# Performance work log

Hardware: AMD Instinct MI355X
Metric: run time of the kernel (lower is better)

## Reference

```python
import jax, jax.numpy as jnp
import numpy as np

N = 50000
E = 800000
C_IN = 32
C_OUT = 32
K = 8  # number of branch MLPs


def setup_inputs() -> dict:
    key = jax.random.key(0)
    ks = jax.random.split(key, 12)
    x = jax.random.normal(ks[0], (N, C_IN), dtype=jnp.float32)
    pos = jax.random.normal(ks[1], (N, 2), dtype=jnp.float32)
    edge_index = jax.random.randint(ks[2], (2, E), 0, N, dtype=jnp.int32)
    edge_attr = jax.random.normal(ks[3], (E, 4), dtype=jnp.float32)
    edge_weight = jax.random.uniform(ks[4], (E,), dtype=jnp.float32)
    s1 = 1.0 / np.sqrt(C_IN + 4)
    s2 = 1.0 / np.sqrt(C_OUT)
    W1 = jax.random.uniform(ks[5], (K, C_IN + 4, C_OUT), jnp.float32, -s1, s1)
    b1 = jax.random.uniform(ks[6], (K, C_OUT), jnp.float32, -s1, s1)
    W2 = jax.random.uniform(ks[7], (K, C_OUT, C_OUT), jnp.float32, -s2, s2)
    b2 = jax.random.uniform(ks[8], (K, C_OUT), jnp.float32, -s2, s2)
    sr = 1.0 / np.sqrt(C_IN)
    Wr = jax.random.uniform(ks[9], (C_IN, C_OUT), jnp.float32, -sr, sr)
    br = jax.random.uniform(ks[10], (C_OUT,), jnp.float32, -sr, sr)
    return {"x": x, "pos": pos, "edge_index": edge_index, "edge_attr": edge_attr,
            "edge_weight": edge_weight, "W1": W1, "b1": b1, "W2": W2, "b2": b2,
            "Wr": Wr, "br": br}


def reference(x, pos, edge_index, edge_attr, edge_weight, W1, b1, W2, b2, Wr, br):
    src = edge_index[0]  # j (source / neighbor)
    tgt = edge_index[1]  # i (target / aggregation index)

    # gather per-edge features
    x_i = x[tgt]                      # [E, C_IN]
    x_j = x[src]                      # [E, C_IN]
    diff = pos[src] - pos[tgt]        # [E, 2]

    # geometric branch index in [0, 8)
    con0 = (diff[:, 0] > 0).astype(jnp.int32)
    con1 = (diff[:, 1] > 0).astype(jnp.int32)
    con2 = (jnp.abs(diff[:, 0]) - jnp.abs(diff[:, 1]) > 0).astype(jnp.int32)
    idx = con0 + con1 * 2 + con2 * 4  # [E]

    m = jnp.concatenate([x_j - x_i, edge_attr], axis=1)  # [E, C_IN+4]
    # all 8 branch MLPs (Linear->ReLU->Linear->ReLU), then select per edge
    h = jax.nn.relu(jnp.einsum('ec,kcf->ekf', m, W1) + b1[None])   # [E, K, C_OUT]
    f_all = jax.nn.relu(jnp.einsum('ekf,kfg->ekg', h, W2) + b2[None])
    f = jnp.take_along_axis(f_all, idx[:, None, None], axis=1)[:, 0, :]  # [E, C_OUT]
    f = edge_weight[:, None] * f

    # scatter-mean over target nodes
    seg_sum = jax.ops.segment_sum(f, tgt, num_segments=N)
    counts = jax.ops.segment_sum(jnp.ones((f.shape[0],), f.dtype), tgt, num_segments=N)
    out = seg_sum / jnp.maximum(counts, 1.0)[:, None]

    # skip connection
    out = out + x @ Wr + br
    return out
```

## Files before the change

### kernel.cpp

```cpp
#include <hip/hip_runtime.h>

#define N_NODES 50000
#define N_EDGES 800000
#define K_BR    8
#define BCAP    131072
#define MLP_SLOTS (K_BR * BCAP)
#define SCAN_BLOCKS 196
#define BSTRIDE 1024
#define EPT 8
#define P1_BLOCKS 391
#define RB 128
#define RBE 6250

typedef _Float16 h2 __attribute__((ext_vector_type(2)));
typedef _Float16 half8 __attribute__((ext_vector_type(8)));
typedef float f32x4 __attribute__((ext_vector_type(4)));

#define MFMA(a, b, c) __builtin_amdgcn_mfma_f32_16x16x32_f16((a), (b), (c), 0, 0, 0)

#define VAL_MASK 0x3FFFFFFFu
#define FLG_A    0x40000000u
#define FLG_P    0x80000000u


__device__ __forceinline__ int branch_idx(float dx, float dy) {
    return (dx > 0.0f ? 1 : 0) + (dy > 0.0f ? 2 : 0) +
           ((fabsf(dx) - fabsf(dy)) > 0.0f ? 4 : 0);
}

__device__ __forceinline__ unsigned pk_f16pair(float a, float b) {
    h2 p; p.x = (_Float16)a; p.y = (_Float16)b;
    return __builtin_bit_cast(unsigned, p);
}

__device__ __forceinline__ unsigned short f16bits(float a) {
    _Float16 h = (_Float16)a;
    return __builtin_bit_cast(unsigned short, h);
}

__global__ void __launch_bounds__(256) rank_kernel(
    const int* __restrict__ ei, const float* __restrict__ x,
    const float* __restrict__ W1, const float* __restrict__ W2,
    unsigned short* __restrict__ rankB, unsigned short* __restrict__ cntM,
    unsigned* __restrict__ xh, uint4* __restrict__ w1f4, uint4* __restrict__ w2f4) {
    __shared__ unsigned hist[N_NODES / 2];
    int t = threadIdx.x, b = blockIdx.x;
    for (int i = t; i < N_NODES / 2; i += 256) hist[i] = 0;

    int tid = b * 256 + t;
    if (tid < 2048) {
        int L = tid & 63, fl = tid >> 6;
        int nt = fl & 1, kt = (fl >> 1) & 1, k = fl >> 2;
        int quad = L >> 4, col = L & 15;
        unsigned dw[4];
#pragma unroll
        for (int i = 0; i < 4; ++i) {
            float v0 = 0.0f, v1 = 0.0f;
            int k0 = kt * 32 + quad * 8 + 2 * i;
            if (k0 < 36)     v0 = W1[k * 1152 + k0 * 32 + nt * 16 + col];
            if (k0 + 1 < 36) v1 = W1[k * 1152 + (k0 + 1) * 32 + nt * 16 + col];
            dw[i] = pk_f16pair(v0, v1);
        }
        w1f4[tid] = make_uint4(dw[0], dw[1], dw[2], dw[3]);
    } else if (tid < 3072) {
        int u2 = tid - 2048;
        int L = u2 & 63, fl = u2 >> 6;
        int nt = fl & 1, k = fl >> 1;
        int quad = L >> 4, col = L & 15;
        unsigned dw[4];
#pragma unroll
        for (int i = 0; i < 4; ++i) {
            int k0 = quad * 8 + 2 * i;
            dw[i] = pk_f16pair(W2[k * 1024 + k0 * 32 + nt * 16 + col],
                               W2[k * 1024 + (k0 + 1) * 32 + nt * 16 + col]);
        }
        w2f4[u2] = make_uint4(dw[0], dw[1], dw[2], dw[3]);
    }

    __syncthreads();
    int eb = b * RBE;
    for (int it = 0; it < (RBE + 255) / 256; ++it) {
        int r = it * 256 + t;
        if (r < RBE) {
            int e = eb + r;
            int d = ei[N_EDGES + e];
            unsigned add = (d & 1) ? (1u << 16) : 1u;
            unsigned old = atomicAdd(&hist[d >> 1], add);
            unsigned rk = (d & 1) ? (old >> 16) : (old & 0xFFFFu);
            rankB[e] = (unsigned short)rk;
            float2 xv = ((const float2*)x)[e];
            xh[e] = pk_f16pair(xv.x, xv.y);
        }
    }
    __syncthreads();
    unsigned* cm = (unsigned*)(cntM + (size_t)b * N_NODES);
    for (int i = t; i < N_NODES / 2; i += 256) cm[i] = hist[i];
}

__global__ void colscan_kernel(const unsigned short* __restrict__ cntM,
                               unsigned short* __restrict__ blkBase,
                               int* __restrict__ cnt) {
    int d = blockIdx.x * 256 + threadIdx.x;
    if (d >= N_NODES) return;
    int acc = 0;
#pragma unroll 8
    for (int b = 0; b < RB; ++b) {
        size_t i = (size_t)b * N_NODES + d;
        int v = cntM[i];
        blkBase[i] = (unsigned short)acc;
        acc += v;
    }
    cnt[d] = acc;
}

__global__ void pass1_kernel(const int* __restrict__ ei, const float* __restrict__ pos,
                             const float* __restrict__ ea, const float* __restrict__ ew,
                             const unsigned short* __restrict__ rankB,
                             const unsigned short* __restrict__ blkBase,
                             int* __restrict__ bucketCur,
                             uint4* __restrict__ payload) {
    __shared__ int h[K_BR];
    __shared__ int base[K_BR];
    int t = threadIdx.x;
    if (t < K_BR) h[t] = 0;
    __syncthreads();

    int eBase = blockIdx.x * (256 * EPT);
    int sA[EPT], dA[EPT], krA[EPT], slA[EPT];
#pragma unroll
    for (int it = 0; it < EPT; ++it) {
        int e = eBase + it * 256 + t;
        int s = 0, d = 0, k = 0, rank = 0, slot = 0;
        if (e < N_EDGES) {
            s = ei[e]; d = ei[N_EDGES + e];
            float2 ps2 = ((const float2*)pos)[s];
            float2 pd2 = ((const float2*)pos)[d];
            k = branch_idx(ps2.x - pd2.x, ps2.y - pd2.y);
            rank = atomicAdd(&h[k], 1);
            int bb = e / RBE;
            slot = (int)blkBase[(size_t)bb * N_NODES + d] + (int)rankB[e];
        }
        sA[it] = s; dA[it] = d; krA[it] = (k << 16) | rank; slA[it] = slot;
    }
    __syncthreads();
    if (t < K_BR) base[t] = (h[t] > 0) ? atomicAdd(&bucketCur[t * BSTRIDE], h[t]) : 0;
    __syncthreads();
#pragma unroll
    for (int it = 0; it < EPT; ++it) {
        int e = eBase + it * 256 + t;
        if (e < N_EDGES) {
            int k = krA[it] >> 16, rank = krA[it] & 0xFFFF;
            float4 eav = ((const float4*)ea)[e];
            unsigned ewh = (unsigned)f16bits(ew[e]);
            int idx = (k << 17) + base[k] + rank;
            payload[idx] = make_uint4((unsigned)sA[it] | ((unsigned)dA[it] << 16),
                                      (unsigned)slA[it] | (ewh << 16),
                                      pk_f16pair(eav.x, eav.y),
                                      pk_f16pair(eav.z, eav.w));
        }
    }
}

__global__ void scan_kernel(const int* __restrict__ cnt, unsigned* __restrict__ ps,
                            int* __restrict__ nodeStart) {
    __shared__ int s[256];
    __shared__ int sh_off;
    int t = threadIdx.x, b = blockIdx.x;
    int i = b * 256 + t;
    int v = (i < N_NODES) ? cnt[i] : 0;
    s[t] = v;
    __syncthreads();
#pragma unroll
    for (int off = 1; off < 256; off <<= 1) {
        int tmp = (t >= off) ? s[t - off] : 0;
        __syncthreads();
        s[t] += tmp;
        __syncthreads();
    }
    int excl = s[t] - v;
    if (t == 255)
        atomicExch(&ps[b], (unsigned)s[255] | (b == 0 ? FLG_P : FLG_A));
    if (t == 0) sh_off = 0;
    if (t < 64 && b > 0) {
        int off = 0;
        int base = b - 1;
        for (;;) {
            int idx = base - t;
            unsigned w = 0;
            if (idx >= 0) {
                do { w = atomicOr(&ps[idx], 0u); } while (!(w & (FLG_A | FLG_P)));
            }
            bool isP = (w & FLG_P) != 0;
            unsigned long long pm = __ballot(isP);
            int firstP = pm ? (__ffsll((unsigned long long)pm) - 1) : 64;
            int contrib = (idx >= 0 && t <= firstP) ? (int)(w & VAL_MASK) : 0;
#pragma unroll
            for (int sh = 32; sh > 0; sh >>= 1) contrib += __shfl_down(contrib, sh, 64);
            contrib = __shfl(contrib, 0, 64);
            off += contrib;
            if (firstP < 64 || base - 64 < 0) break;
            base -= 64;
        }
        if (t == 0) sh_off = off;
    }
    __syncthreads();
    if (i < N_NODES) nodeStart[i] = excl + sh_off;
}

__global__ void __launch_bounds__(64) mlp_kernel(
    const uint4* __restrict__ payload,
    const unsigned* __restrict__ xh,
    const uint4* __restrict__ w1f4, const float* __restrict__ b1,
    const uint4* __restrict__ w2f4, const float* __restrict__ b2,
    const int* __restrict__ nodeStart,
    const int* __restrict__ bucketFill,
    unsigned short* __restrict__ fbuf) {
    __shared__ uint4 lds4[656];
    char* mreg = (char*)lds4;
    char* hreg = mreg + 9216;

    int t = blockIdx.x * 64 + threadIdx.x;
    int u = __builtin_amdgcn_readfirstlane(t);
    int k = u >> 17;
    int fill = bucketFill[k * BSTRIDE];
    if ((u & (BCAP - 1)) >= fill) return;
    int rel = t & (BCAP - 1);
    bool valid = rel < fill;
    int idx = (k << 17) + min(rel, fill - 1);

    int L = threadIdx.x;
    int quad = L >> 4, col = L & 15;

    uint4 pl = payload[idx];
    int s = (int)(pl.x & 0xFFFFu);
    int d = (int)(pl.x >> 16);
    _Float16 wh = __builtin_bit_cast(_Float16, (unsigned short)(pl.y >> 16));
    int slot = valid ? (nodeStart[d] + (int)(pl.y & 0xFFFFu)) : 0;

    const uint4* xj = ((const uint4*)xh) + 4 * (size_t)s;
    const uint4* xi = ((const uint4*)xh) + 4 * (size_t)d;
    uint4* mrow = (uint4*)(mreg + L * 144);
#pragma unroll
    for (int q = 0; q < 4; ++q) {
        half8 a8 = __builtin_bit_cast(half8, xj[q]);
        half8 b8 = __builtin_bit_cast(half8, xi[q]);
        half8 d8 = a8 - b8;
        mrow[q] = __builtin_bit_cast(uint4, d8);
    }
    mrow[4] = make_uint4(pl.z, pl.w, 0u, 0u);
    mrow[5] = make_uint4(0u, 0u, 0u, 0u);
    mrow[6] = make_uint4(0u, 0u, 0u, 0u);
    mrow[7] = make_uint4(0u, 0u, 0u, 0u);

    half8 B1[2][2], B2[2];
#pragma unroll
    for (int kt = 0; kt < 2; ++kt)
#pragma unroll
        for (int nt = 0; nt < 2; ++nt)
            B1[kt][nt] = __builtin_bit_cast(half8, w1f4[((k * 2 + kt) * 2 + nt) * 64 + L]);
#pragma unroll
    for (int nt = 0; nt < 2; ++nt)
        B2[nt] = __builtin_bit_cast(half8, w2f4[(k * 2 + nt) * 64 + L]);
    float b1o0 = b1[k * 32 + col],      b1o1 = b1[k * 32 + 16 + col];
    float b2o0 = b2[k * 32 + col],      b2o1 = b2[k * 32 + 16 + col];

#pragma unroll
    for (int mt = 0; mt < 4; ++mt) {
        int arow = mt * 16 + col;
        half8 a0 = __builtin_bit_cast(half8, *(const uint4*)(mreg + arow * 144 + quad * 16));
        half8 a1 = __builtin_bit_cast(half8, *(const uint4*)(mreg + arow * 144 + 64 + quad * 16));
        f32x4 c0 = {b1o0, b1o0, b1o0, b1o0};
        f32x4 c1 = {b1o1, b1o1, b1o1, b1o1};
        c0 = MFMA(a0, B1[0][0], c0);
        c0 = MFMA(a1, B1[1][0], c0);
        c1 = MFMA(a0, B1[0][1], c1);
        c1 = MFMA(a1, B1[1][1], c1);
#pragma unroll
        for (int r = 0; r < 4; ++r) {
            int er = quad * 4 + r;
            *(unsigned short*)(hreg + er * 80 + col * 2)        = f16bits(fmaxf(c0[r], 0.0f));
            *(unsigned short*)(hreg + er * 80 + (16 + col) * 2) = f16bits(fmaxf(c1[r], 0.0f));
        }
        half8 ah = __builtin_bit_cast(half8, *(const uint4*)(hreg + col * 80 + quad * 16));
        f32x4 d0 = {b2o0, b2o0, b2o0, b2o0};
        f32x4 d1 = {b2o1, b2o1, b2o1, b2o1};
        d0 = MFMA(ah, B2[0], d0);
        d1 = MFMA(ah, B2[1], d1);
#pragma unroll
        for (int r = 0; r < 4; ++r) {
            int edge = mt * 16 + quad * 4 + r;
            *(unsigned short*)(mreg + edge * 144 + col * 2)        = f16bits(fmaxf(d0[r], 0.0f));
            *(unsigned short*)(mreg + edge * 144 + (16 + col) * 2) = f16bits(fmaxf(d1[r], 0.0f));
        }
    }

    half8 w8 = {wh, wh, wh, wh, wh, wh, wh, wh};
    uint4* orow = (uint4*)(mreg + L * 144);
    uint4* frow = (uint4*)(fbuf + 32 * (size_t)slot);
#pragma unroll
    for (int q = 0; q < 4; ++q) {
        half8 v8 = __builtin_bit_cast(half8, orow[q]);
        v8 = v8 * w8;
        if (valid) frow[q] = __builtin_bit_cast(uint4, v8);
    }
}

__global__ void agg_kernel(const unsigned short* __restrict__ fbuf,
                           const int* __restrict__ nodeStart, const int* __restrict__ deg,
                           const float* __restrict__ x, const float* __restrict__ Wr,
                           const float* __restrict__ br, float* __restrict__ out) {
    int t = blockIdx.x * blockDim.x + threadIdx.x;
    if (t >= N_NODES * 8) return;
    int n = t >> 3, g8 = t & 7;
    int st = nodeStart[n], dg = deg[n];
    const uint2* fb = (const uint2*)fbuf;
    float a0 = 0.0f, a1 = 0.0f, a2 = 0.0f, a3 = 0.0f;
    for (int j = 0; j < dg; ++j) {
        uint2 uu = fb[(size_t)(st + j) * 8 + g8];
        h2 p01 = __builtin_bit_cast(h2, uu.x);
        h2 p23 = __builtin_bit_cast(h2, uu.y);
        a0 += (float)p01.x;
        a1 += (float)p01.y;
        a2 += (float)p23.x;
        a3 += (float)p23.y;
    }
    float inv = 1.0f / (float)max(dg, 1);
    int o = g8 * 4;
    a0 = a0 * inv + br[o];
    a1 = a1 * inv + br[o + 1];
    a2 = a2 * inv + br[o + 2];
    a3 = a3 * inv + br[o + 3];
    const float* xr = x + 32 * (size_t)n;
#pragma unroll
    for (int c = 0; c < 32; ++c) {
        float xv = xr[c];
        a0 = fmaf(xv, Wr[c * 32 + o], a0);
        a1 = fmaf(xv, Wr[c * 32 + o + 1], a1);
        a2 = fmaf(xv, Wr[c * 32 + o + 2], a2);
        a3 = fmaf(xv, Wr[c * 32 + o + 3], a3);
    }
    float4* o4 = (float4*)(out + 32 * (size_t)n + o);
    *o4 = make_float4(a0, a1, a2, a3);
}

extern "C" void kernel_launch(void* const* d_in, const int* in_sizes, int n_in,
                              void* d_out, int out_size, void* d_ws, size_t ws_size,
                              hipStream_t stream) {
    const float* x   = (const float*)d_in[0];
    const float* pos = (const float*)d_in[1];
    const int*   ei  = (const int*)d_in[2];
    const float* ea  = (const float*)d_in[3];
    const float* ew  = (const float*)d_in[4];
    const float* W1  = (const float*)d_in[5];
    const float* b1  = (const float*)d_in[6];
    const float* W2  = (const float*)d_in[7];
    const float* b2  = (const float*)d_in[8];
    const float* Wr  = (const float*)d_in[9];
    const float* br  = (const float*)d_in[10];
    float* out = (float*)d_out;

    char* ws = (char*)d_ws;
    unsigned short* fbuf = (unsigned short*)(ws + 0);
    uint4* payload  = (uint4*)(ws + 51200000);
    int* cnt        = (int*)(ws + 67977216);
    int* bucketCur  = (int*)(ws + 68177216);
    unsigned* psLb  = (unsigned*)(ws + 68209984);
    int* nodeStart  = (int*)(ws + 68210816);
    uint4* w1f4     = (uint4*)(ws + 68410816);
    uint4* w2f4     = (uint4*)(ws + 68443584);
    unsigned* xh    = (unsigned*)(ws + 68459968);
    unsigned short* rankB   = (unsigned short*)(ws + 71659968);
    unsigned short* cntM    = (unsigned short*)(ws + 73259968);
    unsigned short* blkBase = (unsigned short*)(ws + 86059968);

    hipMemsetAsync(bucketCur, 0, 33568, stream);

    rank_kernel<<<RB, 256, 0, stream>>>(ei, x, W1, W2, rankB, cntM, xh, w1f4, w2f4);
    colscan_kernel<<<SCAN_BLOCKS, 256, 0, stream>>>(cntM, blkBase, cnt);
    scan_kernel<<<SCAN_BLOCKS, 256, 0, stream>>>(cnt, psLb, nodeStart);
    pass1_kernel<<<P1_BLOCKS, 256, 0, stream>>>(ei, pos, ea, ew, rankB, blkBase,
                                                bucketCur, payload);
    mlp_kernel<<<MLP_SLOTS / 64, 64, 0, stream>>>(payload, xh, w1f4, b1, w2f4, b2,
                                                  nodeStart, bucketCur, fbuf);
    agg_kernel<<<(N_NODES * 8 + 255) / 256, 256, 0, stream>>>(fbuf, nodeStart, cnt,
                                                              x, Wr, br, out);
}
```

Before: 203.9 us.

## Load MLP operands directly into MFMA layout via shuffles, drop LDS staging

The MLP kernel no longer stages per-edge input rows and outputs through a 9 KB LDS region. Each lane shuffles in the source and destination indices of its MFMA row and gathers the x slices straight into A-fragment registers. Outputs are scaled by the edge weight in fp32 and written to fbuf from the MFMA accumulator layout as scattered 16-bit stores. Blocks grow to 128 threads (two waves) with a 4-block occupancy hint, so LDS drops to a per-wave h buffer. The aim is higher occupancy and less LDS traffic, at the cost of redundant gathers and less coalesced 2-byte global writes.

```diff
diff --git a/kernel.cpp b/kernel.cpp
--- a/kernel.cpp
+++ b/kernel.cpp
@@ -11,6 +11,7 @@
 #define P1_BLOCKS 391
 #define RB 128
 #define RBE 6250
+
 
 typedef _Float16 h2 __attribute__((ext_vector_type(2)));
 typedef _Float16 half8 __attribute__((ext_vector_type(8)));
@@ -207,7 +208,7 @@
     if (i < N_NODES) nodeStart[i] = excl + sh_off;
 }
 
-__global__ void __launch_bounds__(64) mlp_kernel(
+__global__ void __launch_bounds__(128, 4) mlp_kernel(
     const uint4* __restrict__ payload,
     const unsigned* __restrict__ xh,
     const uint4* __restrict__ w1f4, const float* __restrict__ b1,
@@ -215,11 +216,10 @@
     const int* __restrict__ nodeStart,
     const int* __restrict__ bucketFill,
     unsigned short* __restrict__ fbuf) {
-    __shared__ uint4 lds4[656];
-    char* mreg = (char*)lds4;
-    char* hreg = mreg + 9216;
-
-    int t = blockIdx.x * 64 + threadIdx.x;
+    __shared__ uint4 lds4[164];
+    char* hreg = (char*)lds4 + (threadIdx.x >> 6) * 1312;
+
+    int t = blockIdx.x * 128 + threadIdx.x;
     int u = __builtin_amdgcn_readfirstlane(t);
     int k = u >> 17;
     int fill = bucketFill[k * BSTRIDE];
@@ -228,29 +228,15 @@
     bool valid = rel < fill;
     int idx = (k << 17) + min(rel, fill - 1);
 
-    int L = threadIdx.x;
+    int L = threadIdx.x & 63;
     int quad = L >> 4, col = L & 15;
 
     uint4 pl = payload[idx];
     int s = (int)(pl.x & 0xFFFFu);
     int d = (int)(pl.x >> 16);
-    _Float16 wh = __builtin_bit_cast(_Float16, (unsigned short)(pl.y >> 16));
+    float whf = (float)__builtin_bit_cast(_Float16, (unsigned short)(pl.y >> 16));
     int slot = valid ? (nodeStart[d] + (int)(pl.y & 0xFFFFu)) : 0;
-
-    const uint4* xj = ((const uint4*)xh) + 4 * (size_t)s;
-    const uint4* xi = ((const uint4*)xh) + 4 * (size_t)d;
-    uint4* mrow = (uint4*)(mreg + L * 144);
-#pragma unroll
-    for (int q = 0; q < 4; ++q) {
-        half8 a8 = __builtin_bit_cast(half8, xj[q]);
-        half8 b8 = __builtin_bit_cast(half8, xi[q]);
-        half8 d8 = a8 - b8;
-        mrow[q] = __builtin_bit_cast(uint4, d8);
-    }
-    mrow[4] = make_uint4(pl.z, pl.w, 0u, 0u);
-    mrow[5] = make_uint4(0u, 0u, 0u, 0u);
-    mrow[6] = make_uint4(0u, 0u, 0u, 0u);
-    mrow[7] = make_uint4(0u, 0u, 0u, 0u);
+    int vld = valid ? 1 : 0;
 
     half8 B1[2][2], B2[2];
 #pragma unroll
@@ -266,9 +252,17 @@
 
 #pragma unroll
     for (int mt = 0; mt < 4; ++mt) {
-        int arow = mt * 16 + col;
-        half8 a0 = __builtin_bit_cast(half8, *(const uint4*)(mreg + arow * 144 + quad * 16));
-        half8 a1 = __builtin_bit_cast(half8, *(const uint4*)(mreg + arow * 144 + 64 + quad * 16));
+        int erA = mt * 16 + col;
+        int sA = __shfl(s, erA, 64);
+        int dAi = __shfl(d, erA, 64);
+        unsigned zA = (unsigned)__shfl((int)pl.z, erA, 64);
+        unsigned wA = (unsigned)__shfl((int)pl.w, erA, 64);
+        uint4 xjv = ((const uint4*)xh)[4 * (size_t)sA + quad];
+        uint4 xiv = ((const uint4*)xh)[4 * (size_t)dAi + quad];
+        half8 a0 = __builtin_bit_cast(half8, xjv) - __builtin_bit_cast(half8, xiv);
+        uint4 a1u = make_uint4(quad == 0 ? zA : 0u, quad == 0 ? wA : 0u, 0u, 0u);
+        half8 a1 = __builtin_bit_cast(half8, a1u);
+
         f32x4 c0 = {b1o0, b1o0, b1o0, b1o0};
         f32x4 c1 = {b1o1, b1o1, b1o1, b1o1};
         c0 = MFMA(a0, B1[0][0], c0);
@@ -288,20 +282,18 @@
         d1 = MFMA(ah, B2[1], d1);
 #pragma unroll
         for (int r = 0; r < 4; ++r) {
-            int edge = mt * 16 + quad * 4 + r;
-            *(unsigned short*)(mreg + edge * 144 + col * 2)        = f16bits(fmaxf(d0[r], 0.0f));
-            *(unsigned short*)(mreg + edge * 144 + (16 + col) * 2) = f16bits(fmaxf(d1[r], 0.0f));
-        }
-    }
-
-    half8 w8 = {wh, wh, wh, wh, wh, wh, wh, wh};
-    uint4* orow = (uint4*)(mreg + L * 144);
-    uint4* frow = (uint4*)(fbuf + 32 * (size_t)slot);
-#pragma unroll
-    for (int q = 0; q < 4; ++q) {
-        half8 v8 = __builtin_bit_cast(half8, orow[q]);
-        v8 = v8 * w8;
-        if (valid) frow[q] = __builtin_bit_cast(uint4, v8);
+            int erC = mt * 16 + quad * 4 + r;
+            int slC = __shfl(slot, erC, 64);
+            float wC = __shfl(whf, erC, 64);
+            int vC = __shfl(vld, erC, 64);
+            unsigned short v0 = f16bits(fmaxf(d0[r], 0.0f) * wC);
+            unsigned short v1 = f16bits(fmaxf(d1[r], 0.0f) * wC);
+            if (vC) {
+                unsigned short* orow = fbuf + 32 * (size_t)slC;
+                orow[col] = v0;
+                orow[16 + col] = v1;
+            }
+        }
     }
 }
 
@@ -380,8 +372,8 @@
     scan_kernel<<<SCAN_BLOCKS, 256, 0, stream>>>(cnt, psLb, nodeStart);
     pass1_kernel<<<P1_BLOCKS, 256, 0, stream>>>(ei, pos, ea, ew, rankB, blkBase,
                                                 bucketCur, payload);
-    mlp_kernel<<<MLP_SLOTS / 64, 64, 0, stream>>>(payload, xh, w1f4, b1, w2f4, b2,
-                                                  nodeStart, bucketCur, fbuf);
+    mlp_kernel<<<MLP_SLOTS / 128, 128, 0, stream>>>(payload, xh, w1f4, b1, w2f4, b2,
+                                                    nodeStart, bucketCur, fbuf);
     agg_kernel<<<(N_NODES * 8 + 255) / 256, 256, 0, stream>>>(fbuf, nodeStart, cnt,
                                                               x, Wr, br, out);
 }
```

After: 189.9 us. 1.07x faster.
